# Kernel optimization log

Measured on AMD Instinct MI355X. Metric: run time of the kernel, lower is better.

The kernel has to match this reference:

```python
import jax, jax.numpy as jnp
import numpy as np

B, K, H, W = 16, 32, 28, 28   # batch, set size, image h, image w
HID, OUT = 64, 64             # hid_dim, out_dim
NOPS = 8                      # permutation-equivariant 3->3 pool/broadcast basis ops


def setup_inputs() -> dict:
    key = jax.random.key(0)
    ks = jax.random.split(key, 8)
    def p(k, shape, fan_in):
        return jax.random.normal(k, shape, jnp.float32) / np.float32(np.sqrt(fan_in))
    return dict(
        x=jax.random.normal(ks[0], (B, K, H, W), jnp.float32),
        conv1_w=p(ks[1], (32, 1, 3, 3), 9),
        conv1_b=jnp.zeros((32,), jnp.float32),
        conv2_w=p(ks[2], (64, 32, 3, 3), 32 * 9),
        conv2_b=jnp.zeros((64,), jnp.float32),
        fc_w=p(ks[3], (HID, 64 * 7 * 7), 64 * 7 * 7),
        fc_b=jnp.zeros((HID,), jnp.float32),
        eq_w=p(ks[4], (HID, OUT, NOPS), HID * NOPS),
        eq_b=jnp.zeros((OUT,), jnp.float32),
        out_w=p(ks[5], (1, OUT), OUT),
        out_b=jnp.zeros((1,), jnp.float32),
    )


def _conv2d(x, w, b):
    y = jax.lax.conv_general_dilated(x, w, (1, 1), 'SAME',
                                     dimension_numbers=('NCHW', 'OIHW', 'NCHW'))
    return y + b[None, :, None, None]


def _maxpool2(x):
    return jax.lax.reduce_window(x, -jnp.inf, jax.lax.max,
                                 (1, 1, 2, 2), (1, 1, 2, 2), 'VALID')


def _forward(x, conv1_w, conv1_b, conv2_w, conv2_b, fc_w, fc_b, eq_w, eq_b, out_w, out_b):
    # --- BasicConvNet embed: (B*K, 1, H, W) -> (B*K, HID) ---
    x1 = x.reshape(B * K, 1, H, W)
    h1 = _maxpool2(jax.nn.relu(_conv2d(x1, conv1_w, conv1_b)))   # (B*K, 32, 14, 14)
    h2 = _maxpool2(jax.nn.relu(_conv2d(h1, conv2_w, conv2_b)))   # (B*K, 64, 7, 7)
    feat = jax.nn.relu(h2.reshape(B * K, -1) @ fc_w.T + fc_b)    # (B*K, HID)
    x4 = feat.reshape(B, K, HID)

    # --- triple outer product: (B, HID, K, K, K), no contracted index ---
    x5 = jnp.einsum('bid,bjd,bkd->bdijk', x4, x4, x4)

    # --- SetEq3to3: 8 equivariant pool/broadcast basis ops, contracted with eq_w[d,e,o].
    # Contract each pooled tensor with its slice of eq_w BEFORE broadcasting (same math,
    # avoids materializing 8 full (B,d,K,K,K) op tensors). ---
    m_i  = x5.mean(2)           # (B, d, j, k)
    m_j  = x5.mean(3)           # (B, d, i, k)
    m_k  = x5.mean(4)           # (B, d, i, j)
    m_ij = m_i.mean(2)          # (B, d, k)
    m_ik = m_i.mean(3)          # (B, d, j)
    m_jk = m_j.mean(3)          # (B, d, i)
    m_all = m_ij.mean(2)        # (B, d)

    x6 = (jnp.einsum('bdijk,de->beijk', x5, eq_w[:, :, 0])
          + jnp.einsum('bdjk,de->bejk', m_i, eq_w[:, :, 1])[:, :, None, :, :]
          + jnp.einsum('bdik,de->beik', m_j, eq_w[:, :, 2])[:, :, :, None, :]
          + jnp.einsum('bdij,de->beij', m_k, eq_w[:, :, 3])[:, :, :, :, None]
          + jnp.einsum('bdk,de->bek', m_ij, eq_w[:, :, 4])[:, :, None, None, :]
          + jnp.einsum('bdj,de->bej', m_ik, eq_w[:, :, 5])[:, :, None, :, None]
          + jnp.einsum('bdi,de->bei', m_jk, eq_w[:, :, 6])[:, :, :, None, None]
          + jnp.einsum('bd,de->be', m_all, eq_w[:, :, 7])[:, :, None, None, None]
          + eq_b[None, :, None, None, None])          # (B, OUT, K, K, K)

    # permute to channels-last, relu, pool over (i,j,k), relu, final linear
    x7 = jax.nn.relu(x6.transpose(0, 2, 3, 4, 1))     # (B, K, K, K, OUT)
    x8 = x7.mean(axis=(1, 2, 3))                      # (B, OUT)
    x9 = jax.nn.relu(x8)
    # dropout_prob = 0 -> identity
    return x9 @ out_w.T + out_b                       # (B, 1)


def reference(x, conv1_w, conv1_b, conv2_w, conv2_b, fc_w, fc_b, eq_w, eq_b, out_w, out_b):
    return _forward(x, conv1_w, conv1_b, conv2_w, conv2_b, fc_w, fc_b,
                    eq_w, eq_b, out_w, out_b)
```

## Files before the change

### kernel.cpp

```cpp
#include <hip/hip_runtime.h>
#include <hip/hip_bf16.h>


typedef __attribute__((ext_vector_type(8))) short short8;
typedef __attribute__((ext_vector_type(4))) float f32x4;

__device__ __forceinline__ f32x4 mfma_bf16(short8 a, short8 b, f32x4 c) {
  return __builtin_amdgcn_mfma_f32_16x16x32_bf16(a, b, c, 0, 0, 0);
}

__device__ __forceinline__ unsigned short f2bs(float f) {
  unsigned int u = __float_as_uint(f);
  unsigned int r = u + 0x7fffu + ((u >> 16) & 1u);
  return (unsigned short)(r >> 16);
}
__device__ __forceinline__ unsigned int pk2(float x, float y) {
  union { __hip_bfloat162 h; unsigned int u; } cv;
  cv.h = __float22bfloat162_rn(make_float2(x, y));
  return cv.u;
}
__device__ __forceinline__ void ub8(const short* p, float* f) {
  uint4 u = *(const uint4*)p;
  f[0] = __uint_as_float(u.x << 16); f[1] = __uint_as_float(u.x & 0xffff0000u);
  f[2] = __uint_as_float(u.y << 16); f[3] = __uint_as_float(u.y & 0xffff0000u);
  f[4] = __uint_as_float(u.z << 16); f[5] = __uint_as_float(u.z & 0xffff0000u);
  f[6] = __uint_as_float(u.w << 16); f[7] = __uint_as_float(u.w & 0xffff0000u);
}

__global__ __launch_bounds__(256, 2) void k12_conv(const float* __restrict__ x,
    const float* __restrict__ w1, const float* __restrict__ b1,
    const float* __restrict__ w2, const float* __restrict__ b2,
    short* __restrict__ h2b,
    const float* __restrict__ eqw, float* __restrict__ W7t, short* __restrict__ Wtb,
    const float* __restrict__ fcw, short* __restrict__ fcwb) {
  const int n = blockIdx.x, t = threadIdx.x;
  if (n >= 512) {
    if (n < 520) {
      const int m = n - 512;
      for (int idx = t; idx < 4096; idx += 256) {
        int e = idx >> 6, d = idx & 63;
        float v = eqw[d*512 + e*8 + m];
        if (m == 7) W7t[idx] = v;
        else        Wtb[m*4096 + idx] = (short)f2bs(v);
      }
    } else {
      int base = (n - 520)*12544 + t;
      for (int q = 0; q < 49; ++q) {
        int idx = base + q*256;
        fcwb[idx] = (short)f2bs(fcw[idx]);
      }
    }
    return;
  }
  __shared__ float si[30*30];
  __shared__ float sw[32*9];
  __shared__ float sb[32];
  __shared__ __align__(16) short inT[16*18*40];
  const int wv = t >> 6, l = t & 63, quad = l >> 4, col = l & 15;

  const int c_out = wv*16 + col;
  float w72[72];
  {
    const float4* src = (const float4*)(w2 + c_out*288 + quad*72);
#pragma unroll
    for (int q = 0; q < 18; ++q) {
      float4 v = src[q];
      w72[q*4+0] = v.x; w72[q*4+1] = v.y; w72[q*4+2] = v.z; w72[q*4+3] = v.w;
    }
  }
  union SU { short8 v; unsigned int u[4]; };
  short8 Bq[9];
#pragma unroll
  for (int dd = 0; dd < 9; ++dd) {
    SU b;
#pragma unroll
    for (int q = 0; q < 4; ++q)
      b.u[q] = pk2(w72[(2*q)*9 + dd], w72[(2*q+1)*9 + dd]);
    Bq[dd] = b.v;
  }
  const float bb2 = b2[c_out];

  for (int idx = t; idx < 900; idx += 256) si[idx] = 0.f;
  {
    unsigned int* zp = (unsigned int*)inT;
    for (int idx = t; idx < 5760; idx += 256) zp[idx] = 0u;
  }
  for (int idx = t; idx < 288; idx += 256) sw[idx] = w1[idx];
  if (t < 32) sb[t] = b1[t];
  __syncthreads();
  for (int idx = t; idx < 784; idx += 256) {
    int y = idx / 28, xx = idx - y*28;
    si[(y+1)*30 + xx + 1] = x[n*784 + idx];
  }
  __syncthreads();

  {
    const int cg = t & 7;
    float wreg[4][9], breg[4];
#pragma unroll
    for (int cc = 0; cc < 4; ++cc) {
      breg[cc] = sb[cg*4 + cc];
#pragma unroll
      for (int q = 0; q < 9; ++q) wreg[cc][q] = sw[(cg*4 + cc)*9 + q];
    }
    for (int idx = t; idx < 1568; idx += 256) {
      int pos = idx >> 3;
      int py = pos / 14, px = pos - py*14;
      float pt[4][4];
#pragma unroll
      for (int r = 0; r < 4; ++r)
#pragma unroll
        for (int q = 0; q < 4; ++q)
          pt[r][q] = si[(2*py + r)*30 + 2*px + q];
      float res[4];
#pragma unroll
      for (int cc = 0; cc < 4; ++cc) {
        float best = 0.f;
#pragma unroll
        for (int a = 0; a < 2; ++a)
#pragma unroll
          for (int b3 = 0; b3 < 2; ++b3) {
            float v = breg[cc]
              + wreg[cc][0]*pt[a+0][b3+0] + wreg[cc][1]*pt[a+0][b3+1] + wreg[cc][2]*pt[a+0][b3+2]
              + wreg[cc][3]*pt[a+1][b3+0] + wreg[cc][4]*pt[a+1][b3+1] + wreg[cc][5]*pt[a+1][b3+2]
              + wreg[cc][6]*pt[a+2][b3+0] + wreg[cc][7]*pt[a+2][b3+1] + wreg[cc][8]*pt[a+2][b3+2];
            best = fmaxf(best, v);
          }
        res[cc] = best;
      }
      uint2 pkd;
      pkd.x = pk2(res[0], res[1]);
      pkd.y = pk2(res[2], res[3]);
      *(uint2*)&inT[(py+1)*720 + (px+1)*40 + cg*4] = pkd;
    }
  }
  __syncthreads();

  for (int p = 0; p < 7; ++p) {
    short8 Ar[4][3];
#pragma unroll
    for (int rr = 0; rr < 4; ++rr)
#pragma unroll
      for (int dx = 0; dx < 3; ++dx)
        Ar[rr][dx] = *(const short8*)&inT[(2*p + rr)*720 + (col + dx)*40 + quad*8];
    f32x4 a0 = {0.f,0.f,0.f,0.f}, a1 = {0.f,0.f,0.f,0.f};
#pragma unroll
    for (int dy = 0; dy < 3; ++dy)
#pragma unroll
      for (int dx = 0; dx < 3; ++dx) {
        a0 = mfma_bf16(Ar[dy][dx],     Bq[dy*3 + dx], a0);
        a1 = mfma_bf16(Ar[dy + 1][dx], Bq[dy*3 + dx], a1);
      }
#pragma unroll
    for (int a = 0; a < 2; ++a) {
      int px = quad*2 + a;
      if (px < 7) {
        float m0 = fmaxf(fmaxf(a0[2*a], a0[2*a + 1]), fmaxf(a1[2*a], a1[2*a + 1]));
        h2b[n*3136 + c_out*49 + p*7 + px] = (short)f2bs(fmaxf(m0 + bb2, 0.f));
      }
    }
  }
}

__global__ __launch_bounds__(256) void k3_mfma(const short* __restrict__ h2b,
    const short* __restrict__ fcwb, float* __restrict__ part) {
  const int blk = blockIdx.x, kp = blockIdx.y, t = threadIdx.x;
  const int w = t >> 6, l = t & 63, quad = l >> 4, col = l & 15;
  const int mt = w & 1, nh = w >> 1;
  const int img = blk*32 + mt*16 + col;
  const short* Ap = h2b + img*3136 + kp*224 + quad*8;
  const short* B0 = fcwb + (nh*32 + col)*3136 + kp*224 + quad*8;
  const short* B1 = fcwb + (nh*32 + 16 + col)*3136 + kp*224 + quad*8;
  f32x4 acc0 = {0.f,0.f,0.f,0.f}, acc1 = {0.f,0.f,0.f,0.f};
#pragma unroll
  for (int q = 0; q < 7; ++q) {
    short8 A  = *(const short8*)(Ap + q*32);
    short8 b0 = *(const short8*)(B0 + q*32);
    short8 b1 = *(const short8*)(B1 + q*32);
    acc0 = mfma_bf16(A, b0, acc0);
    acc1 = mfma_bf16(A, b1, acc1);
  }
  const int e0 = nh*32 + col, e1 = e0 + 16;
  const int base = blk*32 + mt*16 + quad*4;
  float* dst = part + kp*32768;
#pragma unroll
  for (int r = 0; r < 4; ++r) {
    dst[(base + r)*64 + e0] = acc0[r];
    dst[(base + r)*64 + e1] = acc1[r];
  }
}

__global__ __launch_bounds__(256) void k4_prep(const float* __restrict__ part,
    const float* __restrict__ fb, const float* __restrict__ W7t,
    const float* __restrict__ eqb, float* __restrict__ feat,
    float* __restrict__ s, float* __restrict__ t7c) {
  __shared__ __align__(16) float sf[2048];
  __shared__ float ss[64];
  const int b = blockIdx.x, t = threadIdx.x;
  for (int v4 = t; v4 < 512; v4 += 256) {
    float4 a = {0.f, 0.f, 0.f, 0.f};
#pragma unroll
    for (int kp = 0; kp < 14; ++kp) {
      float4 p = *(const float4*)&part[kp*32768 + b*2048 + v4*4];
      a.x += p.x; a.y += p.y; a.z += p.z; a.w += p.w;
    }
    float4 fbv = *(const float4*)&fb[(v4*4) & 63];
    float4 r;
    r.x = fmaxf(a.x + fbv.x, 0.f);
    r.y = fmaxf(a.y + fbv.y, 0.f);
    r.z = fmaxf(a.z + fbv.z, 0.f);
    r.w = fmaxf(a.w + fbv.w, 0.f);
    *(float4*)&sf[v4*4] = r;
    *(float4*)&feat[b*2048 + v4*4] = r;
  }
  __syncthreads();
  if (t < 64) {
    float a = 0.f;
    for (int i = 0; i < 32; ++i) a += sf[i*64 + t];
    a *= (1.f/32.f);
    s[b*64 + t] = a;
    ss[t] = a;
  }
  __syncthreads();
  if (t < 64) {
    const float* W7 = W7t + t*64;
    float t7 = 0.f;
    for (int d = 0; d < 64; ++d) {
      float sv = ss[d];
      t7 += sv*sv*sv * W7[d];
    }
    t7c[b*64 + t] = t7 + eqb[t];
  }
}

__global__ __launch_bounds__(256, 2) void k5_mfma(const float* __restrict__ feat,
    const float* __restrict__ s_, const short* __restrict__ Wtb,
    const float* __restrict__ t7c, float* __restrict__ x8p) {
  __shared__ __align__(16) float Fm[32*68];
  __shared__ __align__(16) float FI[64];
  __shared__ __align__(16) float SV[64];
  __shared__ __align__(16) float C0[64];
  __shared__ float C0P[128];
  __shared__ __align__(16) float KCt[64*36];
  __shared__ float JCf[32*68];
  __shared__ float RED[256];
  __shared__ __align__(16) short Fb[32*72];
  __shared__ __align__(16) short QPb[64*72];
  __shared__ __align__(16) short G2b[64*72];
  __shared__ __align__(16) short G3b[64*72];

  const int i = blockIdx.x, b = blockIdx.y, t = threadIdx.x;
  const int w = t >> 6, l = t & 63, quad = l >> 4, col = l & 15;

  for (int idx = t; idx < 2048; idx += 256) {
    int r = idx >> 6, d = idx & 63;
    float v = feat[b*2048 + idx];
    Fm[r*68 + d] = v;
    Fb[r*72 + d] = (short)f2bs(v);
  }
  if (t < 64) { FI[t] = feat[b*2048 + i*64 + t]; SV[t] = s_[b*64 + t]; }
  __syncthreads();

  {
    const int e = t >> 2, dbase = (t & 3) * 16;
#pragma unroll
    for (int h = 0; h < 2; ++h) {
      int off = dbase + h*8;
      float w0[8], w1[8], w2[8], w3[8], w4[8], w5[8];
      ub8(&Wtb[0*4096 + e*64 + off], w0);
      ub8(&Wtb[1*4096 + e*64 + off], w1);
      ub8(&Wtb[2*4096 + e*64 + off], w2);
      ub8(&Wtb[3*4096 + e*64 + off], w3);
      ub8(&Wtb[4*4096 + e*64 + off], w4);
      ub8(&Wtb[5*4096 + e*64 + off], w5);
      uint4 qv, g2v, g3v;
      unsigned int* qp = &qv.x;
      unsigned int* g2p = &g2v.x;
      unsigned int* g3p = &g3v.x;
#pragma unroll
      for (int j = 0; j < 4; ++j) {
        float fi0 = FI[off + 2*j],     fi1 = FI[off + 2*j + 1];
        float s0  = SV[off + 2*j],     s1  = SV[off + 2*j + 1];
        float q0 = fi0*w0[2*j]   + s0*w1[2*j];
        float q1 = fi1*w0[2*j+1] + s1*w1[2*j+1];
        float a0 = s0*(fi0*w2[2*j]   + s0*w4[2*j]);
        float a1 = s1*(fi1*w2[2*j+1] + s1*w4[2*j+1]);
        float c0 = s0*(fi0*w3[2*j]   + s0*w5[2*j]);
        float c1 = s1*(fi1*w3[2*j+1] + s1*w5[2*j+1]);
        qp[j]  = pk2(q0, q1);
        g2p[j] = pk2(a0, a1);
        g3p[j] = pk2(c0, c1);
      }
      *(uint4*)&QPb[e*72 + off] = qv;
      *(uint4*)&G2b[e*72 + off] = g2v;
      *(uint4*)&G3b[e*72 + off] = g3v;
    }
  }
  if (t < 128) {
    int e = t & 63, dh = t >> 6;
    const short* W6 = Wtb + 6*4096 + e*64 + dh*32;
    float a = 0.f;
#pragma unroll
    for (int g = 0; g < 4; ++g) {
      float wf[8];
      ub8(&W6[g*8], wf);
#pragma unroll
      for (int dd = 0; dd < 8; ++dd) {
        int d = dh*32 + g*8 + dd;
        float sd = SV[d];
        a += sd*sd*FI[d]*wf[dd];
      }
    }
    C0P[dh*64 + e] = a;
  }
  __syncthreads();

  if (w < 2) {
    const short* G = w ? G3b : G2b;
    short8 Bf[4][2];
#pragma unroll
    for (int n = 0; n < 4; ++n)
#pragma unroll
      for (int s2 = 0; s2 < 2; ++s2)
        Bf[n][s2] = *(const short8*)&G[(n*16 + col)*72 + s2*32 + quad*8];
#pragma unroll
    for (int m = 0; m < 2; ++m) {
      short8 A0 = *(const short8*)&Fb[(m*16 + col)*72 + quad*8];
      short8 A1 = *(const short8*)&Fb[(m*16 + col)*72 + 32 + quad*8];
#pragma unroll
      for (int n = 0; n < 4; ++n) {
        f32x4 z = {0.f, 0.f, 0.f, 0.f};
        f32x4 ac = mfma_bf16(A1, Bf[n][1], mfma_bf16(A0, Bf[n][0], z));
        if (w == 0) {
#pragma unroll
          for (int r = 0; r < 4; ++r)
            KCt[(n*16 + col)*36 + m*16 + quad*4 + r] = ac[r];
        } else {
#pragma unroll
          for (int r = 0; r < 4; ++r)
            JCf[(m*16 + quad*4 + r)*68 + n*16 + col] = ac[r];
        }
      }
    }
  } else if (w == 2) {
    C0[l] = C0P[l] + C0P[64 + l] + t7c[b*64 + l];
  }
  __syncthreads();

  float c0v[4];
#pragma unroll
  for (int n = 0; n < 4; ++n) c0v[n] = C0[n*16 + col];
  short8 Bq[4][2];
#pragma unroll
  for (int n = 0; n < 4; ++n)
#pragma unroll
    for (int s2 = 0; s2 < 2; ++s2)
      Bq[n][s2] = *(const short8*)&QPb[(n*16 + col)*72 + s2*32 + quad*8];

  float4 fkv[2][4];
#pragma unroll
  for (int kb2 = 0; kb2 < 2; ++kb2) {
    const float* fk = &Fm[(kb2*16 + col)*68 + quad*8];
    fkv[kb2][0] = *(const float4*)(fk);
    fkv[kb2][1] = *(const float4*)(fk + 4);
    fkv[kb2][2] = *(const float4*)(fk + 32);
    fkv[kb2][3] = *(const float4*)(fk + 36);
  }

  float sum[4] = {0.f, 0.f, 0.f, 0.f};
  union SU { short8 v; unsigned int u[4]; };

#pragma unroll
  for (int jj = 0; jj < 8; ++jj) {
    const int j = w*8 + jj;
    float jc[4];
#pragma unroll
    for (int n = 0; n < 4; ++n) jc[n] = JCf[j*68 + n*16 + col] + c0v[n];
    const float* fj = &Fm[j*68 + quad*8];
    float4 j0 = *(const float4*)(fj);
    float4 j1 = *(const float4*)(fj + 4);
    float4 j2 = *(const float4*)(fj + 32);
    float4 j3 = *(const float4*)(fj + 36);
#pragma unroll
    for (int kb2 = 0; kb2 < 2; ++kb2) {
      float4 k0 = fkv[kb2][0], k1 = fkv[kb2][1];
      float4 k2v = fkv[kb2][2], k3v = fkv[kb2][3];
      SU A0, A1;
      A0.u[0] = pk2(j0.x*k0.x, j0.y*k0.y);
      A0.u[1] = pk2(j0.z*k0.z, j0.w*k0.w);
      A0.u[2] = pk2(j1.x*k1.x, j1.y*k1.y);
      A0.u[3] = pk2(j1.z*k1.z, j1.w*k1.w);
      A1.u[0] = pk2(j2.x*k2v.x, j2.y*k2v.y);
      A1.u[1] = pk2(j2.z*k2v.z, j2.w*k2v.w);
      A1.u[2] = pk2(j3.x*k3v.x, j3.y*k3v.y);
      A1.u[3] = pk2(j3.z*k3v.z, j3.w*k3v.w);
#pragma unroll
      for (int n = 0; n < 4; ++n) {
        f32x4 z = {0.f, 0.f, 0.f, 0.f};
        f32x4 ac = mfma_bf16(A1.v, Bq[n][1], mfma_bf16(A0.v, Bq[n][0], z));
        float4 kc = *(const float4*)&KCt[(n*16 + col)*36 + kb2*16 + quad*4];
        sum[n] += fmaxf(ac[0] + kc.x + jc[n], 0.f);
        sum[n] += fmaxf(ac[1] + kc.y + jc[n], 0.f);
        sum[n] += fmaxf(ac[2] + kc.z + jc[n], 0.f);
        sum[n] += fmaxf(ac[3] + kc.w + jc[n], 0.f);
      }
    }
  }

#pragma unroll
  for (int n = 0; n < 4; ++n) {
    float v = sum[n];
    v += __shfl_xor(v, 16, 64);
    v += __shfl_xor(v, 32, 64);
    if (l < 16) RED[w*64 + n*16 + l] = v;
  }
  __syncthreads();
  if (t < 64) {
    float tot = RED[t] + RED[64 + t] + RED[128 + t] + RED[192 + t];
    x8p[(b*32 + i)*64 + t] = tot;
  }
}

__global__ __launch_bounds__(64) void k6_out(const float* __restrict__ x8p,
    const float* __restrict__ ow, const float* __restrict__ ob,
    float* __restrict__ out) {
  const int bb = blockIdx.x, t = threadIdx.x;
  float a = 0.f;
#pragma unroll
  for (int i = 0; i < 32; ++i) a += x8p[(bb*32 + i)*64 + t];
  float v = fmaxf(a * (1.f/32768.f), 0.f) * ow[t];
#pragma unroll
  for (int off = 32; off > 0; off >>= 1) v += __shfl_down(v, off, 64);
  if (t == 0) out[bb] = v + ob[0];
}

extern "C" void kernel_launch(void* const* d_in, const int* in_sizes, int n_in,
                              void* d_out, int out_size, void* d_ws, size_t ws_size,
                              hipStream_t stream) {
  const float* x   = (const float*)d_in[0];
  const float* c1w = (const float*)d_in[1];
  const float* c1b = (const float*)d_in[2];
  const float* c2w = (const float*)d_in[3];
  const float* c2b = (const float*)d_in[4];
  const float* fcw = (const float*)d_in[5];
  const float* fcb = (const float*)d_in[6];
  const float* eqw = (const float*)d_in[7];
  const float* eqb = (const float*)d_in[8];
  const float* ow  = (const float*)d_in[9];
  const float* ob  = (const float*)d_in[10];
  float* out = (float*)d_out;

  short* h2b  = (short*)d_ws;
  float* feat = (float*)(h2b + 512*3136);
  float* s    = feat + 32768;
  float* t7c  = s + 1024;
  float* x8p  = t7c + 1024;
  float* W7t  = x8p + 32768;
  short* Wtb  = (short*)(W7t + 4096);
  short* fcwb = Wtb + 7*4096;
  float* part = (float*)(fcwb + 200704);

  hipLaunchKernelGGL(k12_conv, dim3(536), dim3(256), 0, stream,
                     x, c1w, c1b, c2w, c2b, h2b, eqw, W7t, Wtb, fcw, fcwb);
  hipLaunchKernelGGL(k3_mfma,  dim3(16, 14), dim3(256), 0, stream, h2b, fcwb, part);
  hipLaunchKernelGGL(k4_prep,  dim3(16),  dim3(256), 0, stream,
                     part, fcb, W7t, eqb, feat, s, t7c);
  hipLaunchKernelGGL(k5_mfma,  dim3(32, 16), dim3(256), 0, stream, feat, s, Wtb, t7c, x8p);
  hipLaunchKernelGGL(k6_out,   dim3(16),  dim3(64),  0, stream, x8p, ow, ob, out);
}
```

Baseline: 124.5 us.

## Stage pairwise feature products through shared memory for MFMA A operands

Instead of each lane computing its own bf16 products F_j*F_k in registers for the MFMA A fragments, the block cooperatively builds tiles of the j,k product matrix (4 j values by 32 k) in a shared buffer aliased onto the G2b/G3b scratch. Each wave then loads its A fragments from that buffer. This cuts per-lane register pressure and spreads the product and bf16 conversion work evenly across threads. In exchange it adds two block barriers per group (16 in total) plus extra LDS write and read traffic.

```diff
diff --git a/kernel.cpp b/kernel.cpp
--- a/kernel.cpp
+++ b/kernel.cpp
@@ -246,11 +246,13 @@
   __shared__ float RED[256];
   __shared__ __align__(16) short Fb[32*72];
   __shared__ __align__(16) short QPb[64*72];
-  __shared__ __align__(16) short G2b[64*72];
-  __shared__ __align__(16) short G3b[64*72];
+  __shared__ __align__(16) short Gbuf[9216];
 
   const int i = blockIdx.x, b = blockIdx.y, t = threadIdx.x;
   const int w = t >> 6, l = t & 63, quad = l >> 4, col = l & 15;
+  short* G2b = Gbuf;
+  short* G3b = Gbuf + 4608;
+  short* PTt = Gbuf;
 
   for (int idx = t; idx < 2048; idx += 256) {
     int r = idx >> 6, d = idx & 63;
@@ -356,48 +358,35 @@
 #pragma unroll
     for (int s2 = 0; s2 < 2; ++s2)
       Bq[n][s2] = *(const short8*)&QPb[(n*16 + col)*72 + s2*32 + quad*8];
-
-  float4 fkv[2][4];
-#pragma unroll
-  for (int kb2 = 0; kb2 < 2; ++kb2) {
-    const float* fk = &Fm[(kb2*16 + col)*68 + quad*8];
-    fkv[kb2][0] = *(const float4*)(fk);
-    fkv[kb2][1] = *(const float4*)(fk + 4);
-    fkv[kb2][2] = *(const float4*)(fk + 32);
-    fkv[kb2][3] = *(const float4*)(fk + 36);
-  }
-
   float sum[4] = {0.f, 0.f, 0.f, 0.f};
-  union SU { short8 v; unsigned int u[4]; };
-
-#pragma unroll
-  for (int jj = 0; jj < 8; ++jj) {
-    const int j = w*8 + jj;
-    float jc[4];
-#pragma unroll
-    for (int n = 0; n < 4; ++n) jc[n] = JCf[j*68 + n*16 + col] + c0v[n];
-    const float* fj = &Fm[j*68 + quad*8];
-    float4 j0 = *(const float4*)(fj);
-    float4 j1 = *(const float4*)(fj + 4);
-    float4 j2 = *(const float4*)(fj + 32);
-    float4 j3 = *(const float4*)(fj + 36);
-#pragma unroll
-    for (int kb2 = 0; kb2 < 2; ++kb2) {
-      float4 k0 = fkv[kb2][0], k1 = fkv[kb2][1];
-      float4 k2v = fkv[kb2][2], k3v = fkv[kb2][3];
-      SU A0, A1;
-      A0.u[0] = pk2(j0.x*k0.x, j0.y*k0.y);
-      A0.u[1] = pk2(j0.z*k0.z, j0.w*k0.w);
-      A0.u[2] = pk2(j1.x*k1.x, j1.y*k1.y);
-      A0.u[3] = pk2(j1.z*k1.z, j1.w*k1.w);
-      A1.u[0] = pk2(j2.x*k2v.x, j2.y*k2v.y);
-      A1.u[1] = pk2(j2.z*k2v.z, j2.w*k2v.w);
-      A1.u[2] = pk2(j3.x*k3v.x, j3.y*k3v.y);
-      A1.u[3] = pk2(j3.z*k3v.z, j3.w*k3v.w);
+
+  for (int g = 0; g < 8; ++g) {
+    for (int lin = t; lin < 2048; lin += 256) {
+      int row = lin >> 4, dg = lin & 15;
+      int jr = g*4 + (row >> 5);
+      int kr = row & 31;
+      float4 fa = *(const float4*)&Fm[jr*68 + dg*4];
+      float4 fbv = *(const float4*)&Fm[kr*68 + dg*4];
+      uint2 p;
+      p.x = pk2(fa.x*fbv.x, fa.y*fbv.y);
+      p.y = pk2(fa.z*fbv.z, fa.w*fbv.w);
+      *(uint2*)&PTt[row*72 + dg*4] = p;
+    }
+    __syncthreads();
+#pragma unroll
+    for (int u = 0; u < 2; ++u) {
+      const int mtl = w*2 + u;
+      const int j = g*4 + (mtl >> 1);
+      const int kb2 = mtl & 1;
+      short8 A0 = *(const short8*)&PTt[(mtl*16 + col)*72 + quad*8];
+      short8 A1 = *(const short8*)&PTt[(mtl*16 + col)*72 + 32 + quad*8];
+      float jc[4];
+#pragma unroll
+      for (int n = 0; n < 4; ++n) jc[n] = JCf[j*68 + n*16 + col] + c0v[n];
 #pragma unroll
       for (int n = 0; n < 4; ++n) {
         f32x4 z = {0.f, 0.f, 0.f, 0.f};
-        f32x4 ac = mfma_bf16(A1.v, Bq[n][1], mfma_bf16(A0.v, Bq[n][0], z));
+        f32x4 ac = mfma_bf16(A1, Bq[n][1], mfma_bf16(A0, Bq[n][0], z));
         float4 kc = *(const float4*)&KCt[(n*16 + col)*36 + kb2*16 + quad*4];
         sum[n] += fmaxf(ac[0] + kc.x + jc[n], 0.f);
         sum[n] += fmaxf(ac[1] + kc.y + jc[n], 0.f);
@@ -405,6 +394,7 @@
         sum[n] += fmaxf(ac[3] + kc.w + jc[n], 0.f);
       }
     }
+    __syncthreads();
   }
 
 #pragma unroll
```

Measured after the change: 124.4 us (median of 2 runs). About the same (-0.1%).
